# Optimization experiments

Hardware: AMD Instinct MI355X
Metric: run time of the kernel (lower is better)

The kernel has to match this reference:

```python
import jax, jax.numpy as jnp
import numpy as np

DIM = 64

def conv2d_g2(x, w, b):
    # 3x3 conv, padding=1, groups=2, NCHW
    y = jax.lax.conv_general_dilated(x, w, (1, 1), [(1, 1), (1, 1)],
                                     dimension_numbers=('NCHW', 'OIHW', 'NCHW'),
                                     feature_group_count=2)
    return y + b[None, :, None, None]

def bilinear_gather(x, py, px):
    # x: [B,C,H,W]; py,px: [B,K,H,W] float sample coords -> [B,K,H,W,C]
    B, C, H, W = x.shape
    y0 = jnp.floor(py); x0 = jnp.floor(px)
    ly = py - y0; lx = px - x0
    hy = 1.0 - ly; hx = 1.0 - lx
    b_idx = jnp.arange(B)[:, None, None, None]
    def gather(yi, xi):
        valid = (yi >= 0) & (yi < H) & (xi >= 0) & (xi < W)
        yc = jnp.clip(yi, 0, H - 1).astype(jnp.int32)
        xc = jnp.clip(xi, 0, W - 1).astype(jnp.int32)
        v = x[b_idx, :, yc, xc]  # [B,K,H,W,C]
        return v * valid[..., None].astype(x.dtype)
    return (gather(y0, x0) * (hy * hx)[..., None]
            + gather(y0, x0 + 1) * (hy * lx)[..., None]
            + gather(y0 + 1, x0) * (ly * hx)[..., None]
            + gather(y0 + 1, x0 + 1) * (ly * lx)[..., None])

def deform_dw(x, offset, w, b, k, pad, dil):
    # depthwise (groups=C, offset_groups=1) deformable conv, stride 1
    B, C, H, W = x.shape
    K = k * k
    off = offset.reshape(B, K, 2, H, W)  # torchvision layout: (dy,dx) per kernel tap
    ky = jnp.repeat(jnp.arange(k), k).astype(x.dtype)   # [K]
    kx = jnp.tile(jnp.arange(k), k).astype(x.dtype)     # [K]
    base_y = jnp.arange(H, dtype=x.dtype)[None, None, :, None] - pad + dil * ky[None, :, None, None]
    base_x = jnp.arange(W, dtype=x.dtype)[None, None, None, :] - pad + dil * kx[None, :, None, None]
    py = base_y + off[:, :, 0]  # [B,K,H,W]
    px = base_x + off[:, :, 1]
    val = bilinear_gather(x, py, px)  # [B,K,H,W,C]
    return jnp.einsum('bkhwc,ck->bchw', val, w.reshape(C, K)) + b[None, :, None, None]

def lsk_forward(x, w_off3, b_off3, w_off2, b_off2, w7, b7, w5, b5):
    B, C, H, W = x.shape
    offset3 = conv2d_g2(x, w_off3, b_off3)            # [B,98,H,W]
    out1 = deform_dw(x, offset3, w7, b7, 7, 9, 3)     # [B,C,H,W]
    offset2 = conv2d_g2(x, w_off2, b_off2)            # [B,50,H,W]
    out2 = deform_dw(out1, offset2, w5, b5, 5, 6, 3)  # [B,C,H,W]
    feats = jnp.stack([out1, out2], axis=1)           # [B,2,C,H,W]
    gap = feats.mean(axis=(3, 4), keepdims=True)      # [B,2,C,1,1]
    attn = jax.nn.softmax(gap, axis=1)
    return jnp.sum(feats * attn, axis=1)              # [B,C,H,W]

def setup_inputs() -> dict:
    key = jax.random.key(0)
    ks = jax.random.split(key, 9)
    B, C, H, W = 4, DIM, 56, 56
    return {
        'x':      jax.random.normal(ks[0], (B, C, H, W), jnp.float32),
        'w_off3': jax.random.normal(ks[1], (98, C // 2, 3, 3), jnp.float32) * 0.05,
        'b_off3': jax.random.normal(ks[2], (98,), jnp.float32) * 0.05,
        'w_off2': jax.random.normal(ks[3], (50, C // 2, 3, 3), jnp.float32) * 0.05,
        'b_off2': jax.random.normal(ks[4], (50,), jnp.float32) * 0.05,
        'w7':     jax.random.normal(ks[5], (C, 1, 7, 7), jnp.float32) * 0.1,
        'b7':     jax.random.normal(ks[6], (C,), jnp.float32) * 0.05,
        'w5':     jax.random.normal(ks[7], (C, 1, 5, 5), jnp.float32) * 0.1,
        'b5':     jax.random.normal(ks[8], (C,), jnp.float32) * 0.05,
    }

def reference(x, w_off3, b_off3, w_off2, b_off2, w7, b7, w5, b5):
    return lsk_forward(x, w_off3, b_off3, w_off2, b_off2, w7, b7, w5, b5)
```

## Files before the change

### kernel.cpp

```cpp
#include <hip/hip_runtime.h>
#include <hip/hip_fp16.h>
#include <math.h>

#define HH 56
#define WW 56
#define CC 64
#define BB 4
#define HWA (HH*WW)

typedef _Float16 half8_t __attribute__((ext_vector_type(8)));
typedef _Float16 h2_t   __attribute__((ext_vector_type(2)));
typedef float f32x4_t __attribute__((ext_vector_type(4)));

__global__ __launch_bounds__(256)
void k_prep(const float* __restrict__ x,
            const float* __restrict__ w3, const float* __restrict__ w2,
            const float* __restrict__ b3, const float* __restrict__ b2,
            __half2* __restrict__ xp, _Float16* __restrict__ xh,
            _Float16* __restrict__ Wp, float* __restrict__ bbp) {
    int blk = blockIdx.x;
    int tid = threadIdx.x;
    if (blk < BB*56) {
        __shared__ float ld[64*57];
        int b = blk / 56, y = blk % 56;
        for (int i = tid; i < 64*56; i += 256) {
            int c = i / 56, col = i % 56;
            ld[c*57 + col] = x[((size_t)b*CC + c)*HWA + y*WW + col];
        }
        __syncthreads();
        for (int i = tid; i < 57*64; i += 256) {
            int j = i >> 6, c = i & 63;
            float lo = (j > 0)  ? ld[c*57 + j - 1] : 0.f;
            float hi = (j < 56) ? ld[c*57 + j]     : 0.f;
            xp[((size_t)(b*HH + y)*57 + j)*CC + c] = __floats2half2_rn(lo, hi);
        }
        _Float16* dst = xh + (((size_t)(b*2)*56 + y)*58)*32;
        for (int i = tid; i < 2*58*32; i += 256) {
            int g = i / 1856;
            int r = i % 1856;
            int col = r / 32, ic = r % 32;
            float v = 0.f;
            if (col >= 1 && col <= 56) v = ld[(g*32 + ic)*57 + col - 1];
            dst[(size_t)g*56*58*32 + r] = (_Float16)v;
        }
    } else {
        int i = (blk - BB*56)*256 + tid;
        if (i < 46080) {
            int j    = i & 7;
            int lane = (i >> 3) & 63;
            int mt   = (i >> 9) % 5;
            int kt   = (i / 2560) % 9;
            int g    = i / 23040;
            int m  = mt*16 + (lane & 15);
            int ic = (lane >> 4)*8 + j;
            int ky = kt/3, kx = kt%3;
            float v = 0.f;
            if (m < 49)      v = w3[((g*49 + m)*32 + ic)*9 + ky*3 + kx];
            else if (m < 74) v = w2[((g*25 + (m-49))*32 + ic)*9 + ky*3 + kx];
            Wp[i] = (_Float16)v;
        } else if (i < 46080 + 160) {
            int t = i - 46080; int g = t/80, m = t%80;
            float v = 0.f;
            if (m < 49)      v = b3[g*49 + m];
            else if (m < 74) v = b2[g*25 + (m-49)];
            bbp[t] = v;
        }
    }
}

__global__ __launch_bounds__(256)
void k_convmfma(const _Float16* __restrict__ xh, const _Float16* __restrict__ Wp,
                const float* __restrict__ bb,
                float* __restrict__ off3, float* __restrict__ off2) {
    __shared__ _Float16 tile[4][3*18*32];
    int blk = blockIdx.x;
    int iy = blk % 56;
    int g  = (blk / 56) & 1;
    int b  = blk / 112;
    int wv   = threadIdx.y;
    int lane = threadIdx.x;
    int n0 = wv * 16;

    const unsigned int* xs = (const unsigned int*)xh;
    unsigned int* tl = (unsigned int*)&tile[wv][0];
#pragma unroll
    for (int i = 0; i < 14; ++i) {
        int idx = i*64 + lane;
        if (idx < 864) {
            int ic2 = idx & 15;
            int seg = idx >> 4;
            int cl = seg % 18, r = seg / 18;
            int y = iy - 1 + r, col = n0 + cl;
            unsigned int v = 0;
            if (y >= 0 && y < 56 && col < 58)
                v = xs[(((size_t)(b*2+g)*56 + y)*58 + col)*16 + ic2];
            tl[idx] = v;
        }
    }
    __syncthreads();

    int nlo = lane & 15, khi = lane >> 4;
    f32x4_t acc[5];
#pragma unroll
    for (int mt = 0; mt < 5; ++mt) acc[mt] = (f32x4_t){0.f,0.f,0.f,0.f};

    const half8_t* wp8 = (const half8_t*)Wp;
#pragma unroll
    for (int kt = 0; kt < 9; ++kt) {
        int ky = kt/3, kx = kt%3;
        half8_t bfrag = *(const half8_t*)&tile[wv][((ky*18) + nlo + kx)*32 + khi*8];
#pragma unroll
        for (int mt = 0; mt < 5; ++mt) {
            half8_t afrag = wp8[(((size_t)g*9 + kt)*5 + mt)*64 + lane];
            acc[mt] = __builtin_amdgcn_mfma_f32_16x16x32_f16(afrag, bfrag, acc[mt], 0, 0, 0);
        }
    }

    int pixcol = n0 + nlo;
    if (pixcol < 56) {
        int pix = iy*WW + pixcol;
#pragma unroll
        for (int mt = 0; mt < 5; ++mt) {
#pragma unroll
            for (int r = 0; r < 4; ++r) {
                int m = mt*16 + khi*4 + r;
                if (m < 74) {
                    float val = acc[mt][r] + bb[g*80 + m];
                    if (m < 49)
                        off3[((size_t)b*98 + g*49 + m)*HWA + pix] = val;
                    else
                        off2[((size_t)b*50 + g*25 + (m-49))*HWA + pix] = val;
                }
            }
        }
    }
}

template<int K, int KS, int PAD, bool WP>
__global__ void k_deform(const h2_t* __restrict__ xp, const float* __restrict__ off,
                         const float* __restrict__ wg, const float* __restrict__ bias,
                         float* __restrict__ out, float* __restrict__ partial,
                         _Float16* __restrict__ xpo) {
    __shared__ float lw[K*65];
    __shared__ float loffs[2*K][4];
    __shared__ int4  lmeta[4][K];
    __shared__ float red[4][64];
    int tid = threadIdx.x + threadIdx.y*64;
    int blk = blockIdx.x;
    int xcd = blk & 7;
    int idx = blk >> 3;
    int b   = xcd >> 1;
    int hw0 = (xcd & 1)*(HWA/2) + idx*4;

    for (int i = tid; i < K*64; i += 256) {
        int c = i / K, t = i % K;
        lw[t*65 + c] = wg[i];
    }
    if (tid < 2*K) {
        float4 v = *(const float4*)&off[((size_t)b*2*K + tid)*HWA + hw0];
        loffs[tid][0] = v.x; loffs[tid][1] = v.y;
        loffs[tid][2] = v.z; loffs[tid][3] = v.w;
    }
    __syncthreads();
    if (tid < 4*K) {
        int p = tid / K, t = tid % K;
        int hw = hw0 + p;
        int h = hw / WW, w = hw % WW;
        int ky = t / KS, kx = t % KS;
        float py = (float)(h - PAD + 3*ky) + loffs[2*t][p];
        float px = (float)(w - PAD + 3*kx) + loffs[2*t+1][p];
        float y0f = floorf(py), x0f = floorf(px);
        float ly = py - y0f, lx = px - x0f;
        float hy = 1.f - ly, hx = 1.f - lx;
        int y0 = (int)y0f, x0 = (int)x0f;
        int j = x0 + 1;
        bool jv = (j >= 0) && (j <= 56);
        int jc = jv ? j : 0;
        float s0 = ((y0   >= 0) && (y0   < HH) && jv) ? hy : 0.f;
        float s1 = ((y0+1 >= 0) && (y0+1 < HH) && jv) ? ly : 0.f;
        int y0c = min(max(y0,   0), HH-1);
        int y1c = min(max(y0+1, 0), HH-1);
        int4 m;
        m.x = (y0c*57 + jc)*64;
        m.y = (y1c*57 + jc)*64;
        __half2 wa = __floats2half2_rn(s0*hx, s0*lx);
        __half2 wb = __floats2half2_rn(s1*hx, s1*lx);
        m.z = *(int*)&wa;
        m.w = *(int*)&wb;
        lmeta[p][t] = m;
    }
    __syncthreads();

    int yp = threadIdx.y;
    int c  = threadIdx.x;
    const h2_t* xb = xp + (size_t)b*HH*57*CC + c;

    float acc = 0.f;
#pragma unroll 2
    for (int t = 0; t < K; ++t) {
        int4 m = lmeta[yp][t];
        h2_t r0 = xb[m.x];
        h2_t r1 = xb[m.y];
        h2_t wA = *(h2_t*)&m.z;
        h2_t wB = *(h2_t*)&m.w;
        float v = __builtin_amdgcn_fdot2(r0, wA, 0.f, false);
        v = __builtin_amdgcn_fdot2(r1, wB, v, false);
        acc = fmaf(v, lw[t*65 + c], acc);
    }
    float val = acc + bias[c];
    int hw = hw0 + yp;
    out[((size_t)b*HWA + hw)*CC + c] = val;

    if (WP) {
        int y = hw / WW, w = hw % WW;
        _Float16* base = xpo + ((size_t)(b*HH + y)*57)*CC*2;
        _Float16 hv = (_Float16)val;
        base[((w    )*64 + c)*2 + 1] = hv;
        base[((w + 1)*64 + c)*2 + 0] = hv;
        if (w == 0)  base[(c)*2 + 0] = (_Float16)0.f;
        if (w == 55) base[((56)*64 + c)*2 + 1] = (_Float16)0.f;
    }

    red[yp][c] = val;
    __syncthreads();
    if (yp == 0)
        partial[((size_t)b*(HWA/4) + (hw0 >> 2))*64 + c]
            = red[0][c] + red[1][c] + red[2][c] + red[3][c];
}

__global__ void k_gapA(const float* __restrict__ p1, const float* __restrict__ p2,
                       float* __restrict__ g2) {
    __shared__ float red[4][64];
    int blk = blockIdx.x;
    int chunk = blk % 14;
    int bf    = blk / 14;
    int b     = bf >> 1;
    const float* p = (bf & 1) ? p2 : p1;
    int tid = threadIdx.x;
    int c = tid & 63, s = tid >> 6;
    float sum = 0.f;
#pragma unroll
    for (int i = 0; i < 14; ++i) {
        int j = chunk*56 + s + 4*i;
        sum += p[((size_t)b*(HWA/4) + j)*64 + c];
    }
    red[s][c] = sum;
    __syncthreads();
    if (s == 0)
        g2[((size_t)bf*14 + chunk)*64 + c]
            = red[0][c] + red[1][c] + red[2][c] + red[3][c];
}

__global__ void k_combine(const float* __restrict__ o1, const float* __restrict__ o2,
                          const float* __restrict__ g2, float* __restrict__ out) {
    __shared__ float tile[64][65];
    __shared__ float gsh[2][64];
    int blk = blockIdx.x;
    int b   = blk / (HWA/64);
    int t0  = (blk % (HWA/64)) * 64;
    int tid = threadIdx.x;
    int c = tid & 63, q = tid >> 6;

    if (tid < 128) {
        int f = tid >> 6, cc = tid & 63;
        float s = 0.f;
#pragma unroll
        for (int k = 0; k < 14; ++k)
            s += g2[((size_t)(b*2+f)*14 + k)*64 + cc];
        gsh[f][cc] = s * (1.f/HWA);
    }
    __syncthreads();

    float g1v = gsh[0][c];
    float g2v = gsh[1][c];
    float m  = fmaxf(g1v, g2v);
    float e1 = expf(g1v - m), e2 = expf(g2v - m);
    float a1 = e1 / (e1 + e2), a2 = 1.f - a1;

#pragma unroll
    for (int i = 0; i < 16; ++i) {
        int p = q + 4*i;
        size_t idx = ((size_t)b*HWA + t0 + p)*CC + c;
        tile[p][c] = o1[idx]*a1 + o2[idx]*a2;
    }
    __syncthreads();
    int p2 = tid & 63;
#pragma unroll
    for (int i = 0; i < 16; ++i) {
        int c2 = q + 4*i;
        out[((size_t)b*CC + c2)*HWA + t0 + p2] = tile[p2][c2];
    }
}

extern "C" void kernel_launch(void* const* d_in, const int* in_sizes, int n_in,
                              void* d_out, int out_size, void* d_ws, size_t ws_size,
                              hipStream_t stream) {
    const float* x      = (const float*)d_in[0];
    const float* w_off3 = (const float*)d_in[1];
    const float* b_off3 = (const float*)d_in[2];
    const float* w_off2 = (const float*)d_in[3];
    const float* b_off2 = (const float*)d_in[4];
    const float* w7     = (const float*)d_in[5];
    const float* b7     = (const float*)d_in[6];
    const float* w5     = (const float*)d_in[7];
    const float* b5     = (const float*)d_in[8];
    float* out = (float*)d_out;

    float* ws    = (float*)d_ws;
    float* off3r = ws;
    float* off2r = off3r + 1229312;
    float* out1  = off2r + 627200;
    float* out2  = out1  + 802816;
    float* xp1f  = out2  + 802816;
    float* xp2f  = xp1f  + 817152;
    float* xhf   = xp2f  + 817152;
    float* part1 = xhf   + 415744;
    float* part2 = part1 + 200704;
    float* gpA   = part2 + 200704;
    float* wpf   = gpA   + 7168;
    float* bbp   = wpf   + 23040;
    __half2*  xp1 = (__half2*)xp1f;
    _Float16* xp2h = (_Float16*)xp2f;
    _Float16* xh  = (_Float16*)xhf;
    _Float16* Wp  = (_Float16*)wpf;
    size_t need = (size_t)(1229312 + 627200 + 802816*2 + 817152*2 + 415744
                           + 200704*2 + 7168 + 23040 + 160) * 4;
    if (ws_size < need) return;

    k_prep<<<BB*56 + 181, 256, 0, stream>>>(x, w_off3, w_off2, b_off3, b_off2,
                                            xp1, xh, Wp, bbp);
    k_convmfma<<<BB*2*56, dim3(64,4), 0, stream>>>(xh, Wp, bbp, off3r, off2r);
    k_deform<49,7,9,true><<<BB*(HWA/4), dim3(64,4), 0, stream>>>(
        (const h2_t*)xp1, off3r, w7, b7, out1, part1, xp2h);
    k_deform<25,5,6,false><<<BB*(HWA/4), dim3(64,4), 0, stream>>>(
        (const h2_t*)xp2f, off2r, w5, b5, out2, part2, nullptr);
    k_gapA<<<8*14, 256, 0, stream>>>(part1, part2, gpA);
    k_combine<<<BB*(HWA/64), 256, 0, stream>>>(out1, out2, gpA, out);
}
```

Baseline: 155.6 us.

## Precompute deform sampling metadata in separate kernel and fuse GAP via atomics

Moves the per-pixel bilinear coordinate and weight computation out of the deform kernels into a new k_offmeta kernel. It reads offsets through coalesced 64-pixel tiles and writes int4 metadata to global memory. The deform kernels then read that metadata per tap, take the addresses with readfirstlane and fully unroll the tap loop. The separate GAP reduction kernel is replaced by atomicAdd into a zeroed buffer, and the zeroing is done inside k_prep. This trades a large extra metadata write and read (about 15 MB) and one added launch for removing the serialized in-block metadata phase and the k_gapA launch.

```diff
diff --git a/kernel.cpp b/kernel.cpp
--- a/kernel.cpp
+++ b/kernel.cpp
@@ -17,7 +17,8 @@
             const float* __restrict__ w3, const float* __restrict__ w2,
             const float* __restrict__ b3, const float* __restrict__ b2,
             __half2* __restrict__ xp, _Float16* __restrict__ xh,
-            _Float16* __restrict__ Wp, float* __restrict__ bbp) {
+            _Float16* __restrict__ Wp, float* __restrict__ bbp,
+            float* __restrict__ gap) {
     int blk = blockIdx.x;
     int tid = threadIdx.x;
     if (blk < BB*56) {
@@ -58,12 +59,14 @@
             if (m < 49)      v = w3[((g*49 + m)*32 + ic)*9 + ky*3 + kx];
             else if (m < 74) v = w2[((g*25 + (m-49))*32 + ic)*9 + ky*3 + kx];
             Wp[i] = (_Float16)v;
-        } else if (i < 46080 + 160) {
+        } else if (i < 46240) {
             int t = i - 46080; int g = t/80, m = t%80;
             float v = 0.f;
             if (m < 49)      v = b3[g*49 + m];
             else if (m < 74) v = b2[g*25 + (m-49)];
             bbp[t] = v;
+        } else if (i < 46240 + 512) {
+            gap[i - 46240] = 0.f;
         }
     }
 }
@@ -136,39 +139,25 @@
     }
 }
 
-template<int K, int KS, int PAD, bool WP>
-__global__ void k_deform(const h2_t* __restrict__ xp, const float* __restrict__ off,
-                         const float* __restrict__ wg, const float* __restrict__ bias,
-                         float* __restrict__ out, float* __restrict__ partial,
-                         _Float16* __restrict__ xpo) {
-    __shared__ float lw[K*65];
-    __shared__ float loffs[2*K][4];
-    __shared__ int4  lmeta[4][K];
-    __shared__ float red[4][64];
-    int tid = threadIdx.x + threadIdx.y*64;
-    int blk = blockIdx.x;
-    int xcd = blk & 7;
-    int idx = blk >> 3;
-    int b   = xcd >> 1;
-    int hw0 = (xcd & 1)*(HWA/2) + idx*4;
-
-    for (int i = tid; i < K*64; i += 256) {
-        int c = i / K, t = i % K;
-        lw[t*65 + c] = wg[i];
-    }
-    if (tid < 2*K) {
-        float4 v = *(const float4*)&off[((size_t)b*2*K + tid)*HWA + hw0];
-        loffs[tid][0] = v.x; loffs[tid][1] = v.y;
-        loffs[tid][2] = v.z; loffs[tid][3] = v.w;
-    }
-    __syncthreads();
-    if (tid < 4*K) {
-        int p = tid / K, t = tid % K;
+template<int K, int KS, int PAD>
+__device__ __forceinline__
+void meta_body(const float* __restrict__ off, int4* __restrict__ meta,
+               int blk, int tid, float* tile) {
+    constexpr int R = 2*K;
+    int b = blk / 49;
+    int hw0 = (blk % 49) * 64;
+    for (int i = tid; i < R*64; i += 256) {
+        int row = i >> 6, p = i & 63;
+        tile[row*65 + p] = off[((size_t)b*R + row)*HWA + hw0 + p];
+    }
+    __syncthreads();
+    for (int i = tid; i < 64*K; i += 256) {
+        int p = i / K, t = i % K;
         int hw = hw0 + p;
         int h = hw / WW, w = hw % WW;
         int ky = t / KS, kx = t % KS;
-        float py = (float)(h - PAD + 3*ky) + loffs[2*t][p];
-        float px = (float)(w - PAD + 3*kx) + loffs[2*t+1][p];
+        float py = (float)(h - PAD + 3*ky) + tile[(2*t)*65 + p];
+        float px = (float)(w - PAD + 3*kx) + tile[(2*t+1)*65 + p];
         float y0f = floorf(py), x0f = floorf(px);
         float ly = py - y0f, lx = px - x0f;
         float hy = 1.f - ly, hx = 1.f - lx;
@@ -187,28 +176,62 @@
         __half2 wb = __floats2half2_rn(s1*hx, s1*lx);
         m.z = *(int*)&wa;
         m.w = *(int*)&wb;
-        lmeta[p][t] = m;
+        meta[((size_t)b*HWA + hw)*K + t] = m;
+    }
+}
+
+__global__ __launch_bounds__(256)
+void k_offmeta(const float* __restrict__ off3, const float* __restrict__ off2,
+               int4* __restrict__ m1, int4* __restrict__ m2) {
+    __shared__ float tile[98*65];
+    int blk = blockIdx.x;
+    int tid = threadIdx.x;
+    if (blk < BB*49) meta_body<49,7,9>(off3, m1, blk, tid, tile);
+    else             meta_body<25,5,6>(off2, m2, blk - BB*49, tid, tile);
+}
+
+template<int K, int F, bool WP>
+__global__ __launch_bounds__(256)
+void k_deform(const h2_t* __restrict__ xp, const int4* __restrict__ meta,
+              const float* __restrict__ wg, const float* __restrict__ bias,
+              float* __restrict__ out, float* __restrict__ gap,
+              _Float16* __restrict__ xpo) {
+    __shared__ float lw[K*65];
+    __shared__ float red[4][64];
+    int tid = threadIdx.x + threadIdx.y*64;
+    int blk = blockIdx.x;
+    int xcd = blk & 7;
+    int idx = blk >> 3;
+    int b   = xcd >> 1;
+    int hw0 = (xcd & 1)*(HWA/2) + idx*4;
+
+    for (int i = tid; i < K*64; i += 256) {
+        int c = i / K, t = i % K;
+        lw[t*65 + c] = wg[i];
     }
     __syncthreads();
 
     int yp = threadIdx.y;
     int c  = threadIdx.x;
-    const h2_t* xb = xp + (size_t)b*HH*57*CC + c;
+    int hw = hw0 + yp;
+    const int4* mrow = meta + ((size_t)b*HWA + hw)*K;
+    const h2_t* xpb  = xp + (size_t)b*HH*57*CC;
 
     float acc = 0.f;
-#pragma unroll 2
+#pragma unroll
     for (int t = 0; t < K; ++t) {
-        int4 m = lmeta[yp][t];
-        h2_t r0 = xb[m.x];
-        h2_t r1 = xb[m.y];
-        h2_t wA = *(h2_t*)&m.z;
-        h2_t wB = *(h2_t*)&m.w;
+        int4 mv = mrow[t];
+        int a0 = __builtin_amdgcn_readfirstlane(mv.x);
+        int a1 = __builtin_amdgcn_readfirstlane(mv.y);
+        h2_t wA = *(h2_t*)&mv.z;
+        h2_t wB = *(h2_t*)&mv.w;
+        h2_t r0 = (xpb + a0)[c];
+        h2_t r1 = (xpb + a1)[c];
         float v = __builtin_amdgcn_fdot2(r0, wA, 0.f, false);
         v = __builtin_amdgcn_fdot2(r1, wB, v, false);
         acc = fmaf(v, lw[t*65 + c], acc);
     }
     float val = acc + bias[c];
-    int hw = hw0 + yp;
     out[((size_t)b*HWA + hw)*CC + c] = val;
 
     if (WP) {
@@ -224,35 +247,12 @@
     red[yp][c] = val;
     __syncthreads();
     if (yp == 0)
-        partial[((size_t)b*(HWA/4) + (hw0 >> 2))*64 + c]
-            = red[0][c] + red[1][c] + red[2][c] + red[3][c];
-}
-
-__global__ void k_gapA(const float* __restrict__ p1, const float* __restrict__ p2,
-                       float* __restrict__ g2) {
-    __shared__ float red[4][64];
-    int blk = blockIdx.x;
-    int chunk = blk % 14;
-    int bf    = blk / 14;
-    int b     = bf >> 1;
-    const float* p = (bf & 1) ? p2 : p1;
-    int tid = threadIdx.x;
-    int c = tid & 63, s = tid >> 6;
-    float sum = 0.f;
-#pragma unroll
-    for (int i = 0; i < 14; ++i) {
-        int j = chunk*56 + s + 4*i;
-        sum += p[((size_t)b*(HWA/4) + j)*64 + c];
-    }
-    red[s][c] = sum;
-    __syncthreads();
-    if (s == 0)
-        g2[((size_t)bf*14 + chunk)*64 + c]
-            = red[0][c] + red[1][c] + red[2][c] + red[3][c];
+        atomicAdd(&gap[(b*2 + F)*64 + c],
+                  red[0][c] + red[1][c] + red[2][c] + red[3][c]);
 }
 
 __global__ void k_combine(const float* __restrict__ o1, const float* __restrict__ o2,
-                          const float* __restrict__ g2, float* __restrict__ out) {
+                          const float* __restrict__ gap, float* __restrict__ out) {
     __shared__ float tile[64][65];
     __shared__ float gsh[2][64];
     int blk = blockIdx.x;
@@ -263,11 +263,7 @@
 
     if (tid < 128) {
         int f = tid >> 6, cc = tid & 63;
-        float s = 0.f;
-#pragma unroll
-        for (int k = 0; k < 14; ++k)
-            s += g2[((size_t)(b*2+f)*14 + k)*64 + cc];
-        gsh[f][cc] = s * (1.f/HWA);
+        gsh[f][cc] = gap[(b*2 + f)*64 + cc] * (1.f/HWA);
     }
     __syncthreads();
 
@@ -314,26 +310,28 @@
     float* xp1f  = out2  + 802816;
     float* xp2f  = xp1f  + 817152;
     float* xhf   = xp2f  + 817152;
-    float* part1 = xhf   + 415744;
-    float* part2 = part1 + 200704;
-    float* gpA   = part2 + 200704;
-    float* wpf   = gpA   + 7168;
+    float* m1f   = xhf   + 415744;
+    float* m2f   = m1f   + 2458624;
+    float* gapv  = m2f   + 1254400;
+    float* wpf   = gapv  + 512;
     float* bbp   = wpf   + 23040;
     __half2*  xp1 = (__half2*)xp1f;
     _Float16* xp2h = (_Float16*)xp2f;
     _Float16* xh  = (_Float16*)xhf;
     _Float16* Wp  = (_Float16*)wpf;
+    int4* m1 = (int4*)m1f;
+    int4* m2 = (int4*)m2f;
     size_t need = (size_t)(1229312 + 627200 + 802816*2 + 817152*2 + 415744
-                           + 200704*2 + 7168 + 23040 + 160) * 4;
+                           + 2458624 + 1254400 + 512 + 23040 + 160) * 4;
     if (ws_size < need) return;
 
-    k_prep<<<BB*56 + 181, 256, 0, stream>>>(x, w_off3, w_off2, b_off3, b_off2,
-                                            xp1, xh, Wp, bbp);
+    k_prep<<<BB*56 + 183, 256, 0, stream>>>(x, w_off3, w_off2, b_off3, b_off2,
+                                            xp1, xh, Wp, bbp, gapv);
     k_convmfma<<<BB*2*56, dim3(64,4), 0, stream>>>(xh, Wp, bbp, off3r, off2r);
-    k_deform<49,7,9,true><<<BB*(HWA/4), dim3(64,4), 0, stream>>>(
-        (const h2_t*)xp1, off3r, w7, b7, out1, part1, xp2h);
-    k_deform<25,5,6,false><<<BB*(HWA/4), dim3(64,4), 0, stream>>>(
-        (const h2_t*)xp2f, off2r, w5, b5, out2, part2, nullptr);
-    k_gapA<<<8*14, 256, 0, stream>>>(part1, part2, gpA);
-    k_combine<<<BB*(HWA/64), 256, 0, stream>>>(out1, out2, gpA, out);
-}
+    k_offmeta<<<BB*49*2, 256, 0, stream>>>(off3r, off2r, m1, m2);
+    k_deform<49,0,true><<<BB*(HWA/4), dim3(64,4), 0, stream>>>(
+        (const h2_t*)xp1, m1, w7, b7, out1, gapv, xp2h);
+    k_deform<25,1,false><<<BB*(HWA/4), dim3(64,4), 0, stream>>>(
+        (const h2_t*)xp2f, m2, w5, b5, out2, gapv, nullptr);
+    k_combine<<<BB*(HWA/64), 256, 0, stream>>>(out1, out2, gapv, out);
+}
```

Result: slower. 176.7 us (+13.6%).

## Pack four bilinear corners per pixel so each deform tap needs one load

Applied to the files above, without the earlier changes.

The fp16 horizontal-pair layout of the deform input is replaced by a 57x57 quad layout. Each entry holds all four bilinear corner values for a channel, so every kernel tap does one 8-byte gather instead of two 4-byte gathers. Out-of-range corners are now zeroed through the interpolation weights, no longer by clamping plus border writes. The cost is twice the buffer size and four scattered stores per pixel in the producers. Padding slots of the quad buffer are never explicitly zeroed, so leftover NaN/Inf in the workspace could leak through the zero weights.

```diff
diff --git a/kernel.cpp b/kernel.cpp
--- a/kernel.cpp
+++ b/kernel.cpp
@@ -12,11 +12,13 @@
 typedef _Float16 h2_t   __attribute__((ext_vector_type(2)));
 typedef float f32x4_t __attribute__((ext_vector_type(4)));
 
+#define QSTR (57*57*64)
+
 __global__ __launch_bounds__(256)
 void k_prep(const float* __restrict__ x,
             const float* __restrict__ w3, const float* __restrict__ w2,
             const float* __restrict__ b3, const float* __restrict__ b2,
-            __half2* __restrict__ xp, _Float16* __restrict__ xh,
+            _Float16* __restrict__ xq1, _Float16* __restrict__ xh,
             _Float16* __restrict__ Wp, float* __restrict__ bbp) {
     int blk = blockIdx.x;
     int tid = threadIdx.x;
@@ -28,11 +30,15 @@
             ld[c*57 + col] = x[((size_t)b*CC + c)*HWA + y*WW + col];
         }
         __syncthreads();
-        for (int i = tid; i < 57*64; i += 256) {
-            int j = i >> 6, c = i & 63;
-            float lo = (j > 0)  ? ld[c*57 + j - 1] : 0.f;
-            float hi = (j < 56) ? ld[c*57 + j]     : 0.f;
-            xp[((size_t)(b*HH + y)*57 + j)*CC + c] = __floats2half2_rn(lo, hi);
+        _Float16* xqb = xq1 + (size_t)b*QSTR*4;
+        for (int i = tid; i < 56*64; i += 256) {
+            int w = i >> 6, c = i & 63;
+            _Float16 hv = (_Float16)ld[c*57 + w];
+            size_t i00 = (((size_t)y*57 + w)*64 + c)*4;
+            xqb[i00 + 3] = hv;
+            xqb[i00 + 64*4 + 2] = hv;
+            xqb[i00 + 57*64*4 + 1] = hv;
+            xqb[i00 + 57*64*4 + 64*4 + 0] = hv;
         }
         _Float16* dst = xh + (((size_t)(b*2)*56 + y)*58)*32;
         for (int i = tid; i < 2*58*32; i += 256) {
@@ -58,7 +64,7 @@
             if (m < 49)      v = w3[((g*49 + m)*32 + ic)*9 + ky*3 + kx];
             else if (m < 74) v = w2[((g*25 + (m-49))*32 + ic)*9 + ky*3 + kx];
             Wp[i] = (_Float16)v;
-        } else if (i < 46080 + 160) {
+        } else if (i < 46240) {
             int t = i - 46080; int g = t/80, m = t%80;
             float v = 0.f;
             if (m < 49)      v = b3[g*49 + m];
@@ -137,10 +143,11 @@
 }
 
 template<int K, int KS, int PAD, bool WP>
-__global__ void k_deform(const h2_t* __restrict__ xp, const float* __restrict__ off,
-                         const float* __restrict__ wg, const float* __restrict__ bias,
-                         float* __restrict__ out, float* __restrict__ partial,
-                         _Float16* __restrict__ xpo) {
+__global__ __launch_bounds__(256)
+void k_deform(const uint2* __restrict__ xq, const float* __restrict__ off,
+              const float* __restrict__ wg, const float* __restrict__ bias,
+              float* __restrict__ out, float* __restrict__ partial,
+              _Float16* __restrict__ xqo) {
     __shared__ float lw[K*65];
     __shared__ float loffs[2*K][4];
     __shared__ int4  lmeta[4][K];
@@ -173,18 +180,17 @@
         float ly = py - y0f, lx = px - x0f;
         float hy = 1.f - ly, hx = 1.f - lx;
         int y0 = (int)y0f, x0 = (int)x0f;
-        int j = x0 + 1;
-        bool jv = (j >= 0) && (j <= 56);
-        int jc = jv ? j : 0;
-        float s0 = ((y0   >= 0) && (y0   < HH) && jv) ? hy : 0.f;
-        float s1 = ((y0+1 >= 0) && (y0+1 < HH) && jv) ? ly : 0.f;
-        int y0c = min(max(y0,   0), HH-1);
-        int y1c = min(max(y0+1, 0), HH-1);
+        float s0  = (y0   >= 0 && y0   < HH) ? hy : 0.f;
+        float s1  = (y0+1 >= 0 && y0+1 < HH) ? ly : 0.f;
+        float wx0 = (x0   >= 0 && x0   < WW) ? hx : 0.f;
+        float wx1 = (x0+1 >= 0 && x0+1 < WW) ? lx : 0.f;
+        int ys = min(max(y0 + 1, 0), 56);
+        int j  = min(max(x0 + 1, 0), 56);
         int4 m;
-        m.x = (y0c*57 + jc)*64;
-        m.y = (y1c*57 + jc)*64;
-        __half2 wa = __floats2half2_rn(s0*hx, s0*lx);
-        __half2 wb = __floats2half2_rn(s1*hx, s1*lx);
+        m.x = (ys*57 + j)*64;
+        m.y = 0;
+        __half2 wa = __floats2half2_rn(s0*wx0, s0*wx1);
+        __half2 wb = __floats2half2_rn(s1*wx0, s1*wx1);
         m.z = *(int*)&wa;
         m.w = *(int*)&wb;
         lmeta[p][t] = m;
@@ -193,32 +199,32 @@
 
     int yp = threadIdx.y;
     int c  = threadIdx.x;
-    const h2_t* xb = xp + (size_t)b*HH*57*CC + c;
+    int hw = hw0 + yp;
+    const uint2* xqb = xq + (size_t)b*QSTR;
 
     float acc = 0.f;
 #pragma unroll 2
     for (int t = 0; t < K; ++t) {
         int4 m = lmeta[yp][t];
-        h2_t r0 = xb[m.x];
-        h2_t r1 = xb[m.y];
+        uint2 q = xqb[m.x + c];
         h2_t wA = *(h2_t*)&m.z;
         h2_t wB = *(h2_t*)&m.w;
-        float v = __builtin_amdgcn_fdot2(r0, wA, 0.f, false);
-        v = __builtin_amdgcn_fdot2(r1, wB, v, false);
+        float v = __builtin_amdgcn_fdot2(*(h2_t*)&q.x, wA, 0.f, false);
+        v = __builtin_amdgcn_fdot2(*(h2_t*)&q.y, wB, v, false);
         acc = fmaf(v, lw[t*65 + c], acc);
     }
     float val = acc + bias[c];
-    int hw = hw0 + yp;
     out[((size_t)b*HWA + hw)*CC + c] = val;
 
     if (WP) {
         int y = hw / WW, w = hw % WW;
-        _Float16* base = xpo + ((size_t)(b*HH + y)*57)*CC*2;
+        _Float16* xb = xqo + (size_t)b*QSTR*4;
         _Float16 hv = (_Float16)val;
-        base[((w    )*64 + c)*2 + 1] = hv;
-        base[((w + 1)*64 + c)*2 + 0] = hv;
-        if (w == 0)  base[(c)*2 + 0] = (_Float16)0.f;
-        if (w == 55) base[((56)*64 + c)*2 + 1] = (_Float16)0.f;
+        size_t i00 = (((size_t)y*57 + w)*64 + c)*4;
+        xb[i00 + 3] = hv;
+        xb[i00 + 64*4 + 2] = hv;
+        xb[i00 + 57*64*4 + 1] = hv;
+        xb[i00 + 57*64*4 + 64*4 + 0] = hv;
     }
 
     red[yp][c] = val;
@@ -311,29 +317,29 @@
     float* off2r = off3r + 1229312;
     float* out1  = off2r + 627200;
     float* out2  = out1  + 802816;
-    float* xp1f  = out2  + 802816;
-    float* xp2f  = xp1f  + 817152;
-    float* xhf   = xp2f  + 817152;
+    float* xq1f  = out2  + 802816;
+    float* xq2f  = xq1f  + 1663488;
+    float* xhf   = xq2f  + 1663488;
     float* part1 = xhf   + 415744;
     float* part2 = part1 + 200704;
     float* gpA   = part2 + 200704;
     float* wpf   = gpA   + 7168;
     float* bbp   = wpf   + 23040;
-    __half2*  xp1 = (__half2*)xp1f;
-    _Float16* xp2h = (_Float16*)xp2f;
+    _Float16* xq1 = (_Float16*)xq1f;
+    _Float16* xq2 = (_Float16*)xq2f;
     _Float16* xh  = (_Float16*)xhf;
     _Float16* Wp  = (_Float16*)wpf;
-    size_t need = (size_t)(1229312 + 627200 + 802816*2 + 817152*2 + 415744
+    size_t need = (size_t)(1229312 + 627200 + 802816*2 + 1663488*2 + 415744
                            + 200704*2 + 7168 + 23040 + 160) * 4;
     if (ws_size < need) return;
 
     k_prep<<<BB*56 + 181, 256, 0, stream>>>(x, w_off3, w_off2, b_off3, b_off2,
-                                            xp1, xh, Wp, bbp);
+                                            xq1, xh, Wp, bbp);
     k_convmfma<<<BB*2*56, dim3(64,4), 0, stream>>>(xh, Wp, bbp, off3r, off2r);
     k_deform<49,7,9,true><<<BB*(HWA/4), dim3(64,4), 0, stream>>>(
-        (const h2_t*)xp1, off3r, w7, b7, out1, part1, xp2h);
+        (const uint2*)xq1, off3r, w7, b7, out1, part1, xq2);
     k_deform<25,5,6,false><<<BB*(HWA/4), dim3(64,4), 0, stream>>>(
-        (const h2_t*)xp2f, off2r, w5, b5, out2, part2, nullptr);
+        (const uint2*)xq2, off2r, w5, b5, out2, part2, nullptr);
     k_gapA<<<8*14, 256, 0, stream>>>(part1, part2, gpA);
     k_combine<<<BB*(HWA/64), 256, 0, stream>>>(out1, out2, gpA, out);
 }
```

Result: slower. 162.6 us (+4.5%).
